# Kernel optimization log

Measured on AMD Instinct MI355X. Metric: run time of the kernel, lower is better.

Reference implementation:

```python
import jax, jax.numpy as jnp
import numpy as np

BN_EPS = 1e-3  # keras BatchNormalization default epsilon
NEG_INF = -1e30


def _masked_row_softmax(adjT):
    # tf.sparse.softmax semantics: softmax over NONZERO entries of each row;
    # implicit zeros stay exactly zero.
    mask = adjT != 0
    logits = jnp.where(mask, adjT, NEG_INF)
    p = jax.nn.softmax(logits, axis=-1)
    return jnp.where(mask, p, 0.0)


def _batch_norm(x, gamma, beta):
    # training-mode BN over all axes except channels
    mean = jnp.mean(x, axis=(0, 1), keepdims=True)
    var = jnp.var(x, axis=(0, 1), keepdims=True)
    return (x - mean) * jax.lax.rsqrt(var + BN_EPS) * gamma + beta


def setup_inputs() -> dict:
    key = jax.random.key(0)
    ks = jax.random.split(key, 4)
    B, N, F = 1, 8192, 128
    C0, C1 = 256, 128
    features = jax.random.normal(ks[0], (B, N, F), dtype=jnp.float32)
    adj = jax.random.randint(ks[1], (B, N, N), 0, 2, dtype=jnp.int32)
    kernel_1 = jax.random.normal(ks[2], (F, C0), dtype=jnp.float32) * (1.0 / np.sqrt(F))
    kernel_2 = jax.random.normal(ks[3], (C0, C1), dtype=jnp.float32) * (1.0 / np.sqrt(C0))
    return {
        "features": features,
        "adj": adj,
        "kernel_1": kernel_1,
        "bias_1": jnp.zeros((C0,), jnp.float32),
        "gamma_1": jnp.ones((C0,), jnp.float32),
        "beta_1": jnp.zeros((C0,), jnp.float32),
        "kernel_2": kernel_2,
        "bias_2": jnp.zeros((C1,), jnp.float32),
        "gamma_2": jnp.ones((C1,), jnp.float32),
        "beta_2": jnp.zeros((C1,), jnp.float32),
    }


def reference(features, adj, kernel_1, bias_1, gamma_1, beta_1,
              kernel_2, bias_2, gamma_2, beta_2):
    # fltr transposed: (B, Nr, Np), then sparse softmax over last dim
    adjT = jnp.transpose(adj.astype(jnp.float32), (0, 2, 1))
    w = _masked_row_softmax(adjT)                      # (B, Nr, Np)
    # people -> region aggregation + projection
    region = jnp.matmul(w, features)                   # (B, Nr, F)
    region = jnp.matmul(region, kernel_1) + bias_1     # (B, Nr, C0)
    region = _batch_norm(region, gamma_1, beta_1)
    # region -> people aggregation + projection
    people = jnp.matmul(jnp.transpose(w, (0, 2, 1)), region)  # (B, Np, C0)
    people = jnp.matmul(people, kernel_2) + bias_2             # (B, Np, C1)
    people = _batch_norm(people, gamma_2, beta_2)
    return people
```

## Files before the change

### kernel.cpp

```cpp
#include <hip/hip_runtime.h>
#include <stdint.h>

typedef unsigned int u32;
typedef unsigned short u16;
typedef unsigned long long u64;
typedef __attribute__((ext_vector_type(8))) short short8;
typedef __attribute__((ext_vector_type(4))) float f32x4;

#define N8K 8192

__device__ __forceinline__ float b2f(u16 u) { return __uint_as_float(((u32)u) << 16); }
__device__ __forceinline__ u16 f2b(float f) {
  u32 i = __float_as_uint(f);
  i += 0x7FFFu + ((i >> 16) & 1u);
  return (u16)(i >> 16);
}
__device__ __forceinline__ u32 pkf(float a, float b) { return (u32)f2b(a) | ((u32)f2b(b) << 16); }

__device__ __forceinline__ int dvote(const u16* f16) {
  u16 u = f16[threadIdx.x * 2];
  int e = (u >> 7) & 0xFF;
  return __syncthreads_count((e >= 0x60 && e <= 0x9F) ? 1 : 0) >= 128;
}

__device__ __forceinline__ void gl_lds16(const void* g, void* l) {
  __builtin_amdgcn_global_load_lds(
      (const __attribute__((address_space(1))) u32*)g,
      (__attribute__((address_space(3))) u32*)l, 16, 0, 0);
}

__device__ __forceinline__ void unpack16(u32 b, uint4& o0, uint4& o1) {
  o0.x = ((b & 0x0001u) ? 0x3F80u : 0u) | ((b & 0x0002u) ? 0x3F800000u : 0u);
  o0.y = ((b & 0x0004u) ? 0x3F80u : 0u) | ((b & 0x0008u) ? 0x3F800000u : 0u);
  o0.z = ((b & 0x0010u) ? 0x3F80u : 0u) | ((b & 0x0020u) ? 0x3F800000u : 0u);
  o0.w = ((b & 0x0040u) ? 0x3F80u : 0u) | ((b & 0x0080u) ? 0x3F800000u : 0u);
  o1.x = ((b & 0x0100u) ? 0x3F80u : 0u) | ((b & 0x0200u) ? 0x3F800000u : 0u);
  o1.y = ((b & 0x0400u) ? 0x3F80u : 0u) | ((b & 0x0800u) ? 0x3F800000u : 0u);
  o1.z = ((b & 0x1000u) ? 0x3F80u : 0u) | ((b & 0x2000u) ? 0x3F800000u : 0u);
  o1.w = ((b & 0x4000u) ? 0x3F80u : 0u) | ((b & 0x8000u) ? 0x3F800000u : 0u);
}

#define MFMA_4x4(As_, Bs_, aoff_, boff_)                                         \
  {                                                                              \
    short8 afr[4], bfr[4];                                                       \
    _Pragma("unroll") for (int i_ = 0; i_ < 4; ++i_)                             \
      afr[i_] = *(const short8*)(As_ + aoff_[i_]);                               \
    _Pragma("unroll") for (int j_ = 0; j_ < 4; ++j_)                             \
      bfr[j_] = *(const short8*)(Bs_ + boff_[j_]);                               \
    _Pragma("unroll") for (int i_ = 0; i_ < 4; ++i_)                             \
      _Pragma("unroll") for (int j_ = 0; j_ < 4; ++j_)                           \
        acc[i_][j_] = __builtin_amdgcn_mfma_f32_16x16x32_bf16(                   \
            afr[i_], bfr[j_], acc[i_][j_], 0, 0, 0);                             \
  }

#define ZERO_ACC()                                                               \
  f32x4 acc[4][4];                                                               \
  {                                                                              \
    const f32x4 fz = {0.f, 0.f, 0.f, 0.f};                                       \
    _Pragma("unroll") for (int i_ = 0; i_ < 4; ++i_)                             \
      _Pragma("unroll") for (int j_ = 0; j_ < 4; ++j_) acc[i_][j_] = fz;         \
  }

__global__ void k_prep(const int* __restrict__ adj,
                       const void* __restrict__ featv, const void* __restrict__ K1v,
                       const void* __restrict__ K2v,
                       const void* __restrict__ b1v, const void* __restrict__ g1v,
                       const void* __restrict__ be1v, const void* __restrict__ b2v,
                       const void* __restrict__ g2v, const void* __restrict__ be2v,
                       u32* __restrict__ RB, u32* __restrict__ CB,
                       u16* __restrict__ Ft, u16* __restrict__ K1T, u16* __restrict__ K2T,
                       float* __restrict__ deg, float* __restrict__ par,
                       float* __restrict__ bn1s, float* __restrict__ bn1q,
                       float* __restrict__ bn2s, float* __restrict__ bn2q) {
  __shared__ u32 Ls[64 * 65];
  __shared__ __align__(16) u16 Lf[32 * 136];
  const int b = blockIdx.x, t = threadIdx.x;
  if (b < 16384) {
    const int r0 = (b & 127) << 6, p0 = (b >> 7) << 6;
    const int lr = t >> 4, lc = (t & 15) << 2;
#pragma unroll
    for (int k = 0; k < 4; ++k) {
      int row = k * 16 + lr;
      int4 v = *(const int4*)(adj + (size_t)(p0 + row) * N8K + r0 + lc);
      u32* d = &Ls[row * 65 + lc];
      d[0] = (u32)v.x; d[1] = (u32)v.y; d[2] = (u32)v.z; d[3] = (u32)v.w;
    }
    __syncthreads();
    const int wv = t >> 6, l = t & 63;
#pragma unroll 4
    for (int i = 0; i < 16; ++i) {
      int row = wv * 16 + i;
      u64 m = __ballot(Ls[row * 65 + l] != 0u);
      if (l == 0) *(u64*)(RB + (size_t)(p0 + row) * 256 + (r0 >> 5)) = m;
    }
#pragma unroll 4
    for (int i = 0; i < 16; ++i) {
      int col = wv * 16 + i;
      u64 m = __ballot(Ls[l * 65 + col] != 0u);
      if (l == 0) *(u64*)(CB + (size_t)(r0 + col) * 256 + (p0 >> 5)) = m;
    }
  } else if (b < 16640) {
    const int flag = dvote((const u16*)featv);
    const int bb = b - 16384;
    const int pr = t >> 3, ck = t & 7;
    u16 v[16];
    if (flag) {
      const u16* s = (const u16*)featv + (size_t)(bb * 32 + pr) * 128 + ck * 16;
      *(uint4*)&v[0] = *(const uint4*)(s);
      *(uint4*)&v[8] = *(const uint4*)(s + 8);
    } else {
      const float* s = (const float*)featv + (size_t)(bb * 32 + pr) * 128 + ck * 16;
#pragma unroll
      for (int i = 0; i < 16; ++i) v[i] = f2b(s[i]);
    }
    *(uint4*)(Lf + pr * 136 + ck * 16) = *(uint4*)&v[0];
    *(uint4*)(Lf + pr * 136 + ck * 16 + 8) = *(uint4*)&v[8];
    __syncthreads();
    const int f = t >> 1, h16 = (t & 1) * 16;
    u32 w[8];
#pragma unroll
    for (int i = 0; i < 8; ++i) {
      u16 lo = Lf[(h16 + 2 * i) * 136 + f];
      u16 hi = Lf[(h16 + 2 * i + 1) * 136 + f];
      w[i] = (u32)lo | ((u32)hi << 16);
    }
    u16* d = Ft + (size_t)bb * 4096 + f * 32 + h16;
    *(uint4*)(d) = *(uint4*)&w[0];
    *(uint4*)(d + 8) = *(uint4*)&w[4];
  } else if (b < 16656) {
    const int flag = dvote((const u16*)featv);
    int o = ((b - 16640) * 256 + t) << 3;
    int k0 = o >> 13, c = (o >> 5) & 255, kk = o & 31;
    uint4 w;
    if (flag) {
      const u16* s = (const u16*)K1v + (size_t)(k0 * 32 + kk) * 256 + c;
      w.x = (u32)s[0]    | ((u32)s[256]  << 16);
      w.y = (u32)s[512]  | ((u32)s[768]  << 16);
      w.z = (u32)s[1024] | ((u32)s[1280] << 16);
      w.w = (u32)s[1536] | ((u32)s[1792] << 16);
    } else {
      const float* s = (const float*)K1v + (size_t)(k0 * 32 + kk) * 256 + c;
      w.x = pkf(s[0], s[256]); w.y = pkf(s[512], s[768]);
      w.z = pkf(s[1024], s[1280]); w.w = pkf(s[1536], s[1792]);
    }
    *(uint4*)(K1T + o) = w;
  } else if (b < 16672) {
    const int flag = dvote((const u16*)featv);
    int o = ((b - 16656) * 256 + t) << 3;
    int k0 = o >> 12, c = (o >> 5) & 127, kk = o & 31;
    uint4 w;
    if (flag) {
      const u16* s = (const u16*)K2v + (size_t)(k0 * 32 + kk) * 128 + c;
      w.x = (u32)s[0]   | ((u32)s[128] << 16);
      w.y = (u32)s[256] | ((u32)s[384] << 16);
      w.z = (u32)s[512] | ((u32)s[640] << 16);
      w.w = (u32)s[768] | ((u32)s[896] << 16);
    } else {
      const float* s = (const float*)K2v + (size_t)(k0 * 32 + kk) * 128 + c;
      w.x = pkf(s[0], s[128]); w.y = pkf(s[256], s[384]);
      w.z = pkf(s[512], s[640]); w.w = pkf(s[768], s[896]);
    }
    *(uint4*)(K2T + o) = w;
  } else {
    const int flag = dvote((const u16*)featv);
    if (t < 256) {
      par[t]       = flag ? b2f(((const u16*)b1v)[t])  : ((const float*)b1v)[t];
      par[256 + t] = flag ? b2f(((const u16*)g1v)[t])  : ((const float*)g1v)[t];
      par[512 + t] = flag ? b2f(((const u16*)be1v)[t]) : ((const float*)be1v)[t];
      bn1s[t] = 0.f; bn1q[t] = 0.f;
    }
    if (t < 128) {
      par[768 + t]  = flag ? b2f(((const u16*)b2v)[t])  : ((const float*)b2v)[t];
      par[896 + t]  = flag ? b2f(((const u16*)g2v)[t])  : ((const float*)g2v)[t];
      par[1024 + t] = flag ? b2f(((const u16*)be2v)[t]) : ((const float*)be2v)[t];
      bn2s[t] = 0.f; bn2q[t] = 0.f;
    }
    for (int i = t; i < N8K; i += 256) deg[i] = 0.f;
  }
}

__global__ __launch_bounds__(256, 2)
void k_gemm1(const u32* __restrict__ CB, const u16* __restrict__ Ft,
             float* __restrict__ P1, float* __restrict__ deg, int ksteps) {
  __shared__ __align__(16) u16 As[128 * 32];
  __shared__ __align__(16) u16 Bs[128 * 32];
  __shared__ float degp[128];
  const int t = threadIdx.x, bx = blockIdx.x;
  const int nt = bx & 63, s = bx >> 6;
  const int n0 = nt << 7;
  const int lane = t & 63, wv = t >> 6;
  const int wm = (wv & 1) << 6, wn = (wv >> 1) << 6;
  const int fm = lane & 15, fq = lane >> 4;
  if (t < 128) degp[t] = 0.0f;
  ZERO_ACC();
  int aoff[4], boff[4];
#pragma unroll
  for (int i = 0; i < 4; ++i) aoff[i] = (wm + i * 16 + fm) * 32 + fq * 8;
#pragma unroll
  for (int j = 0; j < 4; ++j) {
    int n = wn + j * 16 + fm;
    boff[j] = n * 32 + ((fq * 8) ^ (((n >> 2) & 3) << 3));
  }
  const int row = t >> 1, h = t & 1;
  const u32* gB = CB + (size_t)(n0 + row) * 256 + s * ksteps;
  const char* gA = (const char*)(Ft + (size_t)s * ksteps * 4096);
  char* lA = (char*)As + ((t >> 6) << 10);
  const int goff = t << 4;
  const int swz = ((row >> 2) & 3) << 3;
  u16* lb0 = Bs + row * 32 + ((h * 16) ^ swz);
  u16* lb1 = Bs + row * 32 + (((h * 16) + 8) ^ swz);
  int cnt = 0;
  for (int ks = 0; ks < ksteps; ++ks) {
    __syncthreads();
    gl_lds16(gA + goff, lA);
    gl_lds16(gA + 4096 + goff, lA + 4096);
    u32 w = gB[ks];
    gA += 8192;
    u32 bits = (w >> (h * 16)) & 0xFFFFu;
    cnt += __popc(bits);
    uint4 o0, o1;
    unpack16(bits, o0, o1);
    *(uint4*)lb0 = o0;
    *(uint4*)lb1 = o1;
    __syncthreads();
    MFMA_4x4(As, Bs, aoff, boff);
  }
  atomicAdd(&degp[row], (float)cnt);
  float* base = P1 + ((size_t)s * N8K + n0) * 128;
#pragma unroll
  for (int i = 0; i < 4; ++i)
#pragma unroll
    for (int j = 0; j < 4; ++j) {
      int r = wn + j * 16 + fm;
      int f = wm + i * 16 + fq * 4;
      *(f32x4*)(base + (size_t)r * 128 + f) = acc[i][j];
    }
  __syncthreads();
  if (t < 128) atomicAdd(&deg[n0 + t], degp[t]);
}

__global__ __launch_bounds__(256, 2)
void k_projf(const float* __restrict__ Psrc, const float* __restrict__ deg,
             const u16* __restrict__ Bt, const float* __restrict__ bias,
             float* __restrict__ Cout, float* __restrict__ bns, float* __restrict__ bnq,
             int nsplit, int ksteps, int Ncols, int useinv) {
  __shared__ __align__(16) u16 As[128 * 32];
  __shared__ __align__(16) u16 Bs[128 * 32];
  const int t = threadIdx.x, bx = blockIdx.x;
  const int ct = bx & 1, mt = (bx >> 1) & 63;
  const int m0 = mt << 7, n0 = ct << 7;
  const int lane = t & 63, wv = t >> 6;
  const int wm = (wv & 1) << 6, wn = (wv >> 1) << 6;
  const int fm = lane & 15, fq = lane >> 4;
  const int K = ksteps << 5;
  ZERO_ACC();
  int aoff[4], boff[4];
#pragma unroll
  for (int i = 0; i < 4; ++i) {
    int m = wm + i * 16 + fm;
    aoff[i] = m * 32 + ((fq * 8) ^ (((m >> 2) & 3) << 3));
  }
#pragma unroll
  for (int j = 0; j < 4; ++j) boff[j] = (wn + j * 16 + fm) * 32 + fq * 8;
  const int row = t >> 1;
  const size_t sstride = (size_t)N8K * K;
  const float* src = Psrc + (size_t)(m0 + row) * K + (t & 1) * 16;
  float inv = 1.0f;
  if (useinv) {
    float d = deg[m0 + row];
    inv = (d > 0.5f) ? 1.0f / d : 0.0f;
  }
  const int swzA = ((t >> 3) & 3) << 3;
  u16* la0 = As + row * 32 + (((t & 1) * 16) ^ swzA);
  u16* la1 = As + row * 32 + ((((t & 1) * 16) + 8) ^ swzA);
  char* lB = (char*)Bs + ((t >> 6) << 10);
  const int goff = t << 4;
  for (int ks = 0; ks < ksteps; ++ks) {
    __syncthreads();
    const char* gB = (const char*)(Bt + ((size_t)ks * Ncols + n0) * 32);
    gl_lds16(gB + goff, lB);
    gl_lds16(gB + 4096 + goff, lB + 4096);
    f32x4 s0 = {0.f, 0.f, 0.f, 0.f}, s1 = s0, s2 = s0, s3 = s0;
    const float* p = src + ks * 32;
    for (int sp = 0; sp < nsplit; ++sp) {
      const f32x4* q = (const f32x4*)(p + sp * sstride);
      s0 += q[0]; s1 += q[1]; s2 += q[2]; s3 += q[3];
    }
    s0 *= inv; s1 *= inv; s2 *= inv; s3 *= inv;
    uint4 w;
    w.x = pkf(s0[0], s0[1]); w.y = pkf(s0[2], s0[3]);
    w.z = pkf(s1[0], s1[1]); w.w = pkf(s1[2], s1[3]);
    *(uint4*)la0 = w;
    w.x = pkf(s2[0], s2[1]); w.y = pkf(s2[2], s2[3]);
    w.z = pkf(s3[0], s3[1]); w.w = pkf(s3[2], s3[3]);
    *(uint4*)la1 = w;
    __syncthreads();
    MFMA_4x4(As, Bs, aoff, boff);
  }
#pragma unroll
  for (int j = 0; j < 4; ++j) {
    int c = n0 + wn + j * 16 + fm;
    float bc = bias[c];
    float t1 = 0.f, t2 = 0.f;
#pragma unroll
    for (int i = 0; i < 4; ++i) {
      int r = m0 + wm + i * 16 + fq * 4;
#pragma unroll
      for (int ii = 0; ii < 4; ++ii) {
        float v = acc[i][j][ii] + bc;
        Cout[(size_t)(r + ii) * Ncols + c] = v;
        t1 += v; t2 += v * v;
      }
    }
    t1 += __shfl_xor(t1, 16); t1 += __shfl_xor(t1, 32);
    t2 += __shfl_xor(t2, 16); t2 += __shfl_xor(t2, 32);
    if (fq == 0) { atomicAdd(&bns[c], t1); atomicAdd(&bnq[c], t2); }
  }
}

__global__ __launch_bounds__(256, 2)
void k_bnH(const float* __restrict__ region1, const float* __restrict__ deg,
           const float* __restrict__ bn1s, const float* __restrict__ bn1q,
           const float* __restrict__ g1, const float* __restrict__ be1,
           const u16* __restrict__ K2T, u16* __restrict__ HT) {
  __shared__ __align__(16) u16 As[128 * 32];
  __shared__ __align__(16) u16 Bs[128 * 32];
  __shared__ float scS[256], shS[256];
  const int t = threadIdx.x, mt = blockIdx.x;
  const int m0 = mt << 7;
  const int lane = t & 63, wv = t >> 6;
  const int wm = (wv & 1) << 6, wn = (wv >> 1) << 6;
  const int fm = lane & 15, fq = lane >> 4;
  {
    float mu = bn1s[t] * (1.0f / 8192.0f);
    float var = bn1q[t] * (1.0f / 8192.0f) - mu * mu;
    float iv = rsqrtf(var + 1e-3f);
    float sc = iv * g1[t];
    scS[t] = sc;
    shS[t] = be1[t] - mu * sc;
  }
  ZERO_ACC();
  int aoff[4], boff[4];
#pragma unroll
  for (int i = 0; i < 4; ++i) {
    int m = wm + i * 16 + fm;
    aoff[i] = m * 32 + ((fq * 8) ^ (((m >> 2) & 3) << 3));
  }
#pragma unroll
  for (int j = 0; j < 4; ++j) boff[j] = (wn + j * 16 + fm) * 32 + fq * 8;
  const int row = t >> 1, half = t & 1;
  float d = deg[m0 + row];
  const float idg = (d > 0.5f) ? 1.0f / d : 0.0f;
  const float* src = region1 + (size_t)(m0 + row) * 256 + half * 16;
  const int swzA = ((t >> 3) & 3) << 3;
  u16* la0 = As + row * 32 + ((half * 16) ^ swzA);
  u16* la1 = As + row * 32 + (((half * 16) + 8) ^ swzA);
  char* lB = (char*)Bs + ((t >> 6) << 10);
  const int goff = t << 4;
  for (int ks = 0; ks < 8; ++ks) {
    __syncthreads();
    const char* gB = (const char*)(K2T + (size_t)ks * 4096);
    gl_lds16(gB + goff, lB);
    gl_lds16(gB + 4096 + goff, lB + 4096);
    const float* p = src + ks * 32;
    const int cb = ks * 32 + half * 16;
    float y[16];
#pragma unroll
    for (int q = 0; q < 4; ++q) {
      f32x4 x = *(const f32x4*)(p + q * 4);
#pragma unroll
      for (int jj = 0; jj < 4; ++jj)
        y[q * 4 + jj] = (x[jj] * scS[cb + q * 4 + jj] + shS[cb + q * 4 + jj]) * idg;
    }
    uint4 w;
    w.x = pkf(y[0], y[1]); w.y = pkf(y[2], y[3]);
    w.z = pkf(y[4], y[5]); w.w = pkf(y[6], y[7]);
    *(uint4*)la0 = w;
    w.x = pkf(y[8], y[9]); w.y = pkf(y[10], y[11]);
    w.z = pkf(y[12], y[13]); w.w = pkf(y[14], y[15]);
    *(uint4*)la1 = w;
    __syncthreads();
    MFMA_4x4(As, Bs, aoff, boff);
  }
#pragma unroll
  for (int i = 0; i < 4; ++i)
#pragma unroll
    for (int j = 0; j < 4; ++j) {
      int c = wn + j * 16 + fm;
      int r = m0 + wm + i * 16 + fq * 4;
      uint2 w;
      w.x = pkf(acc[i][j][0], acc[i][j][1]);
      w.y = pkf(acc[i][j][2], acc[i][j][3]);
      *(uint2*)(HT + (size_t)(r >> 5) * 4096 + c * 32 + (r & 31)) = w;
    }
}

__global__ __launch_bounds__(256, 2)
void k_gemm2(const u32* __restrict__ RB, const u16* __restrict__ HT,
             float* __restrict__ P2, int ksteps) {
  __shared__ __align__(16) u16 As[128 * 32];
  __shared__ __align__(16) u16 Bs[128 * 32];
  const int t = threadIdx.x, bx = blockIdx.x;
  const int mt = bx & 63, s = bx >> 6;
  const int m0 = mt << 7;
  const int lane = t & 63, wv = t >> 6;
  const int wm = (wv & 1) << 6, wn = (wv >> 1) << 6;
  const int fm = lane & 15, fq = lane >> 4;
  ZERO_ACC();
  int aoff[4], boff[4];
#pragma unroll
  for (int i = 0; i < 4; ++i) {
    int m = wm + i * 16 + fm;
    aoff[i] = m * 32 + ((fq * 8) ^ (((m >> 2) & 3) << 3));
  }
#pragma unroll
  for (int j = 0; j < 4; ++j) boff[j] = (wn + j * 16 + fm) * 32 + fq * 8;
  const int row = t >> 1, h = t & 1;
  const u32* gA = RB + (size_t)(m0 + row) * 256 + s * ksteps;
  const char* gB = (const char*)(HT + (size_t)s * ksteps * 4096);
  char* lB = (char*)Bs + ((t >> 6) << 10);
  const int goff = t << 4;
  const int swzA = ((row >> 2) & 3) << 3;
  u16* la0 = As + row * 32 + ((h * 16) ^ swzA);
  u16* la1 = As + row * 32 + (((h * 16) + 8) ^ swzA);
  for (int ks = 0; ks < ksteps; ++ks) {
    __syncthreads();
    gl_lds16(gB + goff, lB);
    gl_lds16(gB + 4096 + goff, lB + 4096);
    u32 w = gA[ks];
    gB += 8192;
    u32 bits = (w >> (h * 16)) & 0xFFFFu;
    uint4 o0, o1;
    unpack16(bits, o0, o1);
    *(uint4*)la0 = o0;
    *(uint4*)la1 = o1;
    __syncthreads();
    MFMA_4x4(As, Bs, aoff, boff);
  }
  float* base = P2 + (size_t)s * N8K * 128;
#pragma unroll
  for (int i = 0; i < 4; ++i)
#pragma unroll
    for (int j = 0; j < 4; ++j) {
      int c = wn + j * 16 + fm;
      int pr = m0 + wm + i * 16 + fq * 4;
#pragma unroll
      for (int ii = 0; ii < 4; ++ii)
        base[(size_t)(pr + ii) * 128 + c] = acc[i][j][ii];
    }
}

__global__ void k_red2(const float* __restrict__ P2, const float* __restrict__ bias,
                       float* __restrict__ people1,
                       float* __restrict__ bn2s, float* __restrict__ bn2q) {
  __shared__ float r1[256], r2[256];
  const int t = threadIdx.x;
  const int c = t & 127, pg = t >> 7;
  const int p0 = blockIdx.x << 5;
  const float bc = bias[c];
  float s1 = 0.f, s2 = 0.f;
  for (int pp = pg; pp < 32; pp += 2) {
    size_t o = (size_t)(p0 + pp) * 128 + c;
    float v = bc;
#pragma unroll
    for (int s = 0; s < 8; ++s) v += P2[(size_t)s * N8K * 128 + o];
    people1[o] = v;
    s1 += v; s2 += v * v;
  }
  r1[t] = s1; r2[t] = s2;
  __syncthreads();
  if (t < 128) {
    atomicAdd(&bn2s[t], r1[t] + r1[t + 128]);
    atomicAdd(&bn2q[t], r2[t] + r2[t + 128]);
  }
}

__global__ void k_bn2apply(const float* __restrict__ people1,
                           const float* __restrict__ bn2s, const float* __restrict__ bn2q,
                           const float* __restrict__ g2, const float* __restrict__ be2,
                           const u16* __restrict__ featprobe, void* __restrict__ outv) {
  const int flag = dvote(featprobe);
  int g = blockIdx.x * 256 + threadIdx.x;
  int p = g >> 5;
  int c = (g & 31) << 2;
  f32x4 x = *(const f32x4*)(people1 + (size_t)p * 128 + c);
  f32x4 y;
#pragma unroll
  for (int jj = 0; jj < 4; ++jj) {
    int cc = c + jj;
    float mu = bn2s[cc] * (1.0f / 8192.0f);
    float var = bn2q[cc] * (1.0f / 8192.0f) - mu * mu;
    float inv = rsqrtf(var + 1e-3f);
    y[jj] = (x[jj] - mu) * inv * g2[cc] + be2[cc];
  }
  if (flag) {
    uint2 w;
    w.x = pkf(y[0], y[1]);
    w.y = pkf(y[2], y[3]);
    *(uint2*)((u16*)outv + (size_t)p * 128 + c) = w;
  } else {
    *(f32x4*)((float*)outv + (size_t)p * 128 + c) = y;
  }
}

extern "C" void kernel_launch(void* const* d_in, const int* in_sizes, int n_in,
                              void* d_out, int out_size, void* d_ws, size_t ws_size,
                              hipStream_t stream) {
  const void* feat = d_in[0];
  const int* adj   = (const int*)d_in[1];
  const void* K1   = d_in[2];
  const void* b1   = d_in[3];
  const void* g1   = d_in[4];
  const void* be1  = d_in[5];
  const void* K2   = d_in[6];
  const void* b2   = d_in[7];
  const void* g2   = d_in[8];
  const void* be2  = d_in[9];
  char* ws = (char*)d_ws;
  const size_t MB = 1u << 20;

  float* Pbig    = (float*)(ws);
  float* region1 = (float*)(ws + 32 * MB);
  float* people1 = (float*)(ws + 40 * MB);
  u16*   Ft      = (u16*)(ws + 44 * MB);
  u16*   HT      = (u16*)(ws + 46 * MB);
  u32*   RB      = (u32*)(ws + 48 * MB);
  u32*   CB      = (u32*)(ws + 56 * MB);
  u16*   K1T     = (u16*)(ws + 64 * MB);
  u16*   K2T     = K1T + 32768;
  float* deg     = (float*)(K2T + 32768);
  float* par     = deg + N8K;
  float* bn1s    = par + 1152;
  float* bn1q    = bn1s + 256;
  float* bn2s    = bn1q + 256;
  float* bn2q    = bn2s + 128;

  k_prep<<<16673, 256, 0, stream>>>(adj, feat, K1, K2, b1, g1, be1, b2, g2, be2,
                                    RB, CB, Ft, K1T, K2T, deg, par,
                                    bn1s, bn1q, bn2s, bn2q);
  k_gemm1<<<512, 256, 0, stream>>>(CB, Ft, Pbig, deg, 32);
  k_projf<<<128, 256, 0, stream>>>(Pbig, deg, K1T, par + 0, region1, bn1s, bn1q,
                                   8, 4, 256, 1);
  k_bnH<<<64, 256, 0, stream>>>(region1, deg, bn1s, bn1q, par + 256, par + 512,
                                K2T, HT);
  k_gemm2<<<512, 256, 0, stream>>>(RB, HT, Pbig, 32);
  k_red2<<<256, 256, 0, stream>>>(Pbig, par + 768, people1, bn2s, bn2q);
  k_bn2apply<<<1024, 256, 0, stream>>>(people1, bn2s, bn2q, par + 896, par + 1024,
                                       (const u16*)feat, d_out);
}
```

Before: 508.1 us.

## Load MFMA fragments directly from global memory, removing LDS staging and barriers

The four GEMM kernels no longer stage A/B tiles through shared memory with double __syncthreads per k-step. Each lane now reads its MFMA fragments straight from global memory, and the adjacency bitmask is unpacked in registers per lane, reading four k-steps of mask words at once. Degree counting moves from shared-memory atomics to per-lane popcounts plus global atomics. This removes barrier and LDS traffic, but each lane now issues more redundant global loads through L1/L2, and load latency is no longer hidden by explicit staging.

```diff
diff --git a/kernel.cpp b/kernel.cpp
--- a/kernel.cpp
+++ b/kernel.cpp
@@ -9,6 +9,8 @@
 
 #define N8K 8192
 
+union U16x8 { uint4 u; short8 s; };
+
 __device__ __forceinline__ float b2f(u16 u) { return __uint_as_float(((u32)u) << 16); }
 __device__ __forceinline__ u16 f2b(float f) {
   u32 i = __float_as_uint(f);
@@ -23,35 +25,20 @@
   return __syncthreads_count((e >= 0x60 && e <= 0x9F) ? 1 : 0) >= 128;
 }
 
-__device__ __forceinline__ void gl_lds16(const void* g, void* l) {
-  __builtin_amdgcn_global_load_lds(
-      (const __attribute__((address_space(1))) u32*)g,
-      (__attribute__((address_space(3))) u32*)l, 16, 0, 0);
-}
-
-__device__ __forceinline__ void unpack16(u32 b, uint4& o0, uint4& o1) {
-  o0.x = ((b & 0x0001u) ? 0x3F80u : 0u) | ((b & 0x0002u) ? 0x3F800000u : 0u);
-  o0.y = ((b & 0x0004u) ? 0x3F80u : 0u) | ((b & 0x0008u) ? 0x3F800000u : 0u);
-  o0.z = ((b & 0x0010u) ? 0x3F80u : 0u) | ((b & 0x0020u) ? 0x3F800000u : 0u);
-  o0.w = ((b & 0x0040u) ? 0x3F80u : 0u) | ((b & 0x0080u) ? 0x3F800000u : 0u);
-  o1.x = ((b & 0x0100u) ? 0x3F80u : 0u) | ((b & 0x0200u) ? 0x3F800000u : 0u);
-  o1.y = ((b & 0x0400u) ? 0x3F80u : 0u) | ((b & 0x0800u) ? 0x3F800000u : 0u);
-  o1.z = ((b & 0x1000u) ? 0x3F80u : 0u) | ((b & 0x2000u) ? 0x3F800000u : 0u);
-  o1.w = ((b & 0x4000u) ? 0x3F80u : 0u) | ((b & 0x8000u) ? 0x3F800000u : 0u);
-}
-
-#define MFMA_4x4(As_, Bs_, aoff_, boff_)                                         \
-  {                                                                              \
-    short8 afr[4], bfr[4];                                                       \
-    _Pragma("unroll") for (int i_ = 0; i_ < 4; ++i_)                             \
-      afr[i_] = *(const short8*)(As_ + aoff_[i_]);                               \
+__device__ __forceinline__ short8 unpack8(u32 b) {
+  U16x8 u;
+  u.u.x = ((b & 0x01u) ? 0x3F80u : 0u) | ((b & 0x02u) ? 0x3F800000u : 0u);
+  u.u.y = ((b & 0x04u) ? 0x3F80u : 0u) | ((b & 0x08u) ? 0x3F800000u : 0u);
+  u.u.z = ((b & 0x10u) ? 0x3F80u : 0u) | ((b & 0x20u) ? 0x3F800000u : 0u);
+  u.u.w = ((b & 0x40u) ? 0x3F80u : 0u) | ((b & 0x80u) ? 0x3F800000u : 0u);
+  return u.s;
+}
+
+#define MFMA_ALL()                                                               \
+  _Pragma("unroll") for (int i_ = 0; i_ < 4; ++i_)                               \
     _Pragma("unroll") for (int j_ = 0; j_ < 4; ++j_)                             \
-      bfr[j_] = *(const short8*)(Bs_ + boff_[j_]);                               \
-    _Pragma("unroll") for (int i_ = 0; i_ < 4; ++i_)                             \
-      _Pragma("unroll") for (int j_ = 0; j_ < 4; ++j_)                           \
-        acc[i_][j_] = __builtin_amdgcn_mfma_f32_16x16x32_bf16(                   \
-            afr[i_], bfr[j_], acc[i_][j_], 0, 0, 0);                             \
-  }
+      acc[i_][j_] = __builtin_amdgcn_mfma_f32_16x16x32_bf16(                     \
+          afr[i_], bfr[j_], acc[i_][j_], 0, 0, 0);
 
 #define ZERO_ACC()                                                               \
   f32x4 acc[4][4];                                                               \
@@ -60,6 +47,11 @@
     _Pragma("unroll") for (int i_ = 0; i_ < 4; ++i_)                             \
       _Pragma("unroll") for (int j_ = 0; j_ < 4; ++j_) acc[i_][j_] = fz;         \
   }
+
+#define LANE_DECODE()                                                            \
+  const int lane = t & 63, wv = t >> 6;                                          \
+  const int wm = (wv & 1) << 6, wn = (wv >> 1) << 6;                             \
+  const int fm = lane & 15, fq = lane >> 4;
 
 __global__ void k_prep(const int* __restrict__ adj,
                        const void* __restrict__ featv, const void* __restrict__ K1v,
@@ -181,51 +173,48 @@
 
 __global__ __launch_bounds__(256, 2)
 void k_gemm1(const u32* __restrict__ CB, const u16* __restrict__ Ft,
-             float* __restrict__ P1, float* __restrict__ deg, int ksteps) {
-  __shared__ __align__(16) u16 As[128 * 32];
-  __shared__ __align__(16) u16 Bs[128 * 32];
-  __shared__ float degp[128];
+             float* __restrict__ P1, float* __restrict__ deg) {
   const int t = threadIdx.x, bx = blockIdx.x;
   const int nt = bx & 63, s = bx >> 6;
   const int n0 = nt << 7;
-  const int lane = t & 63, wv = t >> 6;
-  const int wm = (wv & 1) << 6, wn = (wv >> 1) << 6;
-  const int fm = lane & 15, fq = lane >> 4;
-  if (t < 128) degp[t] = 0.0f;
+  LANE_DECODE();
+  const int sh = fq * 8;
   ZERO_ACC();
-  int aoff[4], boff[4];
-#pragma unroll
-  for (int i = 0; i < 4; ++i) aoff[i] = (wm + i * 16 + fm) * 32 + fq * 8;
-#pragma unroll
-  for (int j = 0; j < 4; ++j) {
-    int n = wn + j * 16 + fm;
-    boff[j] = n * 32 + ((fq * 8) ^ (((n >> 2) & 3) << 3));
-  }
-  const int row = t >> 1, h = t & 1;
-  const u32* gB = CB + (size_t)(n0 + row) * 256 + s * ksteps;
-  const char* gA = (const char*)(Ft + (size_t)s * ksteps * 4096);
-  char* lA = (char*)As + ((t >> 6) << 10);
-  const int goff = t << 4;
-  const int swz = ((row >> 2) & 3) << 3;
-  u16* lb0 = Bs + row * 32 + ((h * 16) ^ swz);
-  u16* lb1 = Bs + row * 32 + (((h * 16) + 8) ^ swz);
-  int cnt = 0;
-  for (int ks = 0; ks < ksteps; ++ks) {
-    __syncthreads();
-    gl_lds16(gA + goff, lA);
-    gl_lds16(gA + 4096 + goff, lA + 4096);
-    u32 w = gB[ks];
-    gA += 8192;
-    u32 bits = (w >> (h * 16)) & 0xFFFFu;
-    cnt += __popc(bits);
-    uint4 o0, o1;
-    unpack16(bits, o0, o1);
-    *(uint4*)lb0 = o0;
-    *(uint4*)lb1 = o1;
-    __syncthreads();
-    MFMA_4x4(As, Bs, aoff, boff);
-  }
-  atomicAdd(&degp[row], (float)cnt);
+  const u16* aP[4];
+#pragma unroll
+  for (int i = 0; i < 4; ++i)
+    aP[i] = Ft + (size_t)s * 32 * 4096 + (wm + i * 16 + fm) * 32 + fq * 8;
+  const u32* bP[4];
+#pragma unroll
+  for (int j = 0; j < 4; ++j)
+    bP[j] = CB + (size_t)(n0 + wn + j * 16 + fm) * 256 + s * 32;
+  u32 cnt[4] = {0u, 0u, 0u, 0u};
+  for (int ks4 = 0; ks4 < 8; ++ks4) {
+    uint4 bw[4];
+#pragma unroll
+    for (int j = 0; j < 4; ++j) bw[j] = *(const uint4*)(bP[j] + ks4 * 4);
+#pragma unroll
+    for (int kk = 0; kk < 4; ++kk) {
+      short8 afr[4], bfr[4];
+#pragma unroll
+      for (int i = 0; i < 4; ++i)
+        afr[i] = *(const short8*)(aP[i] + (ks4 * 4 + kk) * 4096);
+#pragma unroll
+      for (int j = 0; j < 4; ++j) {
+        u32 w = ((const u32*)&bw[j])[kk];
+        bfr[j] = unpack8((w >> sh) & 0xFFu);
+      }
+      MFMA_ALL();
+    }
+#pragma unroll
+    for (int j = 0; j < 4; ++j)
+      cnt[j] += __popc(bw[j].x) + __popc(bw[j].y) + __popc(bw[j].z) + __popc(bw[j].w);
+  }
+  if (((wv & 1) == 0) && fq == 0) {
+#pragma unroll
+    for (int j = 0; j < 4; ++j)
+      atomicAdd(&deg[n0 + wn + j * 16 + fm], (float)cnt[j]);
+  }
   float* base = P1 + ((size_t)s * N8K + n0) * 128;
 #pragma unroll
   for (int i = 0; i < 4; ++i)
@@ -235,67 +224,47 @@
       int f = wm + i * 16 + fq * 4;
       *(f32x4*)(base + (size_t)r * 128 + f) = acc[i][j];
     }
-  __syncthreads();
-  if (t < 128) atomicAdd(&deg[n0 + t], degp[t]);
 }
 
 __global__ __launch_bounds__(256, 2)
-void k_projf(const float* __restrict__ Psrc, const float* __restrict__ deg,
-             const u16* __restrict__ Bt, const float* __restrict__ bias,
-             float* __restrict__ Cout, float* __restrict__ bns, float* __restrict__ bnq,
-             int nsplit, int ksteps, int Ncols, int useinv) {
-  __shared__ __align__(16) u16 As[128 * 32];
-  __shared__ __align__(16) u16 Bs[128 * 32];
+void k_projf(const float* __restrict__ P1, const float* __restrict__ deg,
+             const u16* __restrict__ K1T, const float* __restrict__ bias,
+             float* __restrict__ Cout, float* __restrict__ bns, float* __restrict__ bnq) {
   const int t = threadIdx.x, bx = blockIdx.x;
-  const int ct = bx & 1, mt = (bx >> 1) & 63;
+  const int ct = bx & 1, mt = bx >> 1;
   const int m0 = mt << 7, n0 = ct << 7;
-  const int lane = t & 63, wv = t >> 6;
-  const int wm = (wv & 1) << 6, wn = (wv >> 1) << 6;
-  const int fm = lane & 15, fq = lane >> 4;
-  const int K = ksteps << 5;
+  LANE_DECODE();
   ZERO_ACC();
-  int aoff[4], boff[4];
+  int rowi[4];
+  float idg[4];
 #pragma unroll
   for (int i = 0; i < 4; ++i) {
-    int m = wm + i * 16 + fm;
-    aoff[i] = m * 32 + ((fq * 8) ^ (((m >> 2) & 3) << 3));
-  }
-#pragma unroll
-  for (int j = 0; j < 4; ++j) boff[j] = (wn + j * 16 + fm) * 32 + fq * 8;
-  const int row = t >> 1;
-  const size_t sstride = (size_t)N8K * K;
-  const float* src = Psrc + (size_t)(m0 + row) * K + (t & 1) * 16;
-  float inv = 1.0f;
-  if (useinv) {
-    float d = deg[m0 + row];
-    inv = (d > 0.5f) ? 1.0f / d : 0.0f;
-  }
-  const int swzA = ((t >> 3) & 3) << 3;
-  u16* la0 = As + row * 32 + (((t & 1) * 16) ^ swzA);
-  u16* la1 = As + row * 32 + ((((t & 1) * 16) + 8) ^ swzA);
-  char* lB = (char*)Bs + ((t >> 6) << 10);
-  const int goff = t << 4;
-  for (int ks = 0; ks < ksteps; ++ks) {
-    __syncthreads();
-    const char* gB = (const char*)(Bt + ((size_t)ks * Ncols + n0) * 32);
-    gl_lds16(gB + goff, lB);
-    gl_lds16(gB + 4096 + goff, lB + 4096);
-    f32x4 s0 = {0.f, 0.f, 0.f, 0.f}, s1 = s0, s2 = s0, s3 = s0;
-    const float* p = src + ks * 32;
-    for (int sp = 0; sp < nsplit; ++sp) {
-      const f32x4* q = (const f32x4*)(p + sp * sstride);
-      s0 += q[0]; s1 += q[1]; s2 += q[2]; s3 += q[3];
-    }
-    s0 *= inv; s1 *= inv; s2 *= inv; s3 *= inv;
-    uint4 w;
-    w.x = pkf(s0[0], s0[1]); w.y = pkf(s0[2], s0[3]);
-    w.z = pkf(s1[0], s1[1]); w.w = pkf(s1[2], s1[3]);
-    *(uint4*)la0 = w;
-    w.x = pkf(s2[0], s2[1]); w.y = pkf(s2[2], s2[3]);
-    w.z = pkf(s3[0], s3[1]); w.w = pkf(s3[2], s3[3]);
-    *(uint4*)la1 = w;
-    __syncthreads();
-    MFMA_4x4(As, Bs, aoff, boff);
+    rowi[i] = m0 + wm + i * 16 + fm;
+    float d = deg[rowi[i]];
+    idg[i] = (d > 0.5f) ? 1.0f / d : 0.0f;
+  }
+  for (int ks = 0; ks < 4; ++ks) {
+    short8 afr[4], bfr[4];
+#pragma unroll
+    for (int i = 0; i < 4; ++i) {
+      const float* p = P1 + (size_t)rowi[i] * 128 + ks * 32 + fq * 8;
+      f32x4 s0 = {0.f, 0.f, 0.f, 0.f}, s1 = s0;
+#pragma unroll
+      for (int sp = 0; sp < 8; ++sp) {
+        const float* q = p + (size_t)sp * N8K * 128;
+        s0 += *(const f32x4*)(q);
+        s1 += *(const f32x4*)(q + 4);
+      }
+      s0 *= idg[i]; s1 *= idg[i];
+      U16x8 u;
+      u.u.x = pkf(s0[0], s0[1]); u.u.y = pkf(s0[2], s0[3]);
+      u.u.z = pkf(s1[0], s1[1]); u.u.w = pkf(s1[2], s1[3]);
+      afr[i] = u.s;
+    }
+#pragma unroll
+    for (int j = 0; j < 4; ++j)
+      bfr[j] = *(const short8*)(K1T + ((size_t)ks * 256 + n0 + wn + j * 16 + fm) * 32 + fq * 8);
+    MFMA_ALL();
   }
 #pragma unroll
   for (int j = 0; j < 4; ++j) {
@@ -308,7 +277,7 @@
 #pragma unroll
       for (int ii = 0; ii < 4; ++ii) {
         float v = acc[i][j][ii] + bc;
-        Cout[(size_t)(r + ii) * Ncols + c] = v;
+        Cout[(size_t)(r + ii) * 256 + c] = v;
         t1 += v; t2 += v * v;
       }
     }
@@ -323,14 +292,10 @@
            const float* __restrict__ bn1s, const float* __restrict__ bn1q,
            const float* __restrict__ g1, const float* __restrict__ be1,
            const u16* __restrict__ K2T, u16* __restrict__ HT) {
-  __shared__ __align__(16) u16 As[128 * 32];
-  __shared__ __align__(16) u16 Bs[128 * 32];
   __shared__ float scS[256], shS[256];
   const int t = threadIdx.x, mt = blockIdx.x;
   const int m0 = mt << 7;
-  const int lane = t & 63, wv = t >> 6;
-  const int wm = (wv & 1) << 6, wn = (wv >> 1) << 6;
-  const int fm = lane & 15, fq = lane >> 4;
+  LANE_DECODE();
   {
     float mu = bn1s[t] * (1.0f / 8192.0f);
     float var = bn1q[t] * (1.0f / 8192.0f) - mu * mu;
@@ -339,48 +304,41 @@
     scS[t] = sc;
     shS[t] = be1[t] - mu * sc;
   }
+  __syncthreads();
   ZERO_ACC();
-  int aoff[4], boff[4];
+  int rowi[4];
+  float idg[4];
 #pragma unroll
   for (int i = 0; i < 4; ++i) {
-    int m = wm + i * 16 + fm;
-    aoff[i] = m * 32 + ((fq * 8) ^ (((m >> 2) & 3) << 3));
-  }
-#pragma unroll
-  for (int j = 0; j < 4; ++j) boff[j] = (wn + j * 16 + fm) * 32 + fq * 8;
-  const int row = t >> 1, half = t & 1;
-  float d = deg[m0 + row];
-  const float idg = (d > 0.5f) ? 1.0f / d : 0.0f;
-  const float* src = region1 + (size_t)(m0 + row) * 256 + half * 16;
-  const int swzA = ((t >> 3) & 3) << 3;
-  u16* la0 = As + row * 32 + ((half * 16) ^ swzA);
-  u16* la1 = As + row * 32 + (((half * 16) + 8) ^ swzA);
-  char* lB = (char*)Bs + ((t >> 6) << 10);
-  const int goff = t << 4;
+    rowi[i] = m0 + wm + i * 16 + fm;
+    float d = deg[rowi[i]];
+    idg[i] = (d > 0.5f) ? 1.0f / d : 0.0f;
+  }
   for (int ks = 0; ks < 8; ++ks) {
-    __syncthreads();
-    const char* gB = (const char*)(K2T + (size_t)ks * 4096);
-    gl_lds16(gB + goff, lB);
-    gl_lds16(gB + 4096 + goff, lB + 4096);
-    const float* p = src + ks * 32;
-    const int cb = ks * 32 + half * 16;
-    float y[16];
-#pragma unroll
-    for (int q = 0; q < 4; ++q) {
-      f32x4 x = *(const f32x4*)(p + q * 4);
-#pragma unroll
-      for (int jj = 0; jj < 4; ++jj)
-        y[q * 4 + jj] = (x[jj] * scS[cb + q * 4 + jj] + shS[cb + q * 4 + jj]) * idg;
-    }
-    uint4 w;
-    w.x = pkf(y[0], y[1]); w.y = pkf(y[2], y[3]);
-    w.z = pkf(y[4], y[5]); w.w = pkf(y[6], y[7]);
-    *(uint4*)la0 = w;
-    w.x = pkf(y[8], y[9]); w.y = pkf(y[10], y[11]);
-    w.z = pkf(y[12], y[13]); w.w = pkf(y[14], y[15]);
-    *(uint4*)la1 = w;
-    __syncthreads();
-    MFMA_4x4(As, Bs, aoff, boff);
+    const int c0 = ks * 32 + fq * 8;
+    float sc[8], shf[8];
+#pragma unroll
+    for (int jj = 0; jj < 8; ++jj) { sc[jj] = scS[c0 + jj]; shf[jj] = shS[c0 + jj]; }
+    short8 afr[4], bfr[4];
+#pragma unroll
+    for (int i = 0; i < 4; ++i) {
+      const float* p = region1 + (size_t)rowi[i] * 256 + c0;
+      f32x4 x0 = *(const f32x4*)(p);
+      f32x4 x1 = *(const f32x4*)(p + 4);
+      float y[8];
+#pragma unroll
+      for (int jj = 0; jj < 4; ++jj) y[jj] = (x0[jj] * sc[jj] + shf[jj]) * idg[i];
+#pragma unroll
+      for (int jj = 0; jj < 4; ++jj) y[4 + jj] = (x1[jj] * sc[4 + jj] + shf[4 + jj]) * idg[i];
+      U16x8 u;
+      u.u.x = pkf(y[0], y[1]); u.u.y = pkf(y[2], y[3]);
+      u.u.z = pkf(y[4], y[5]); u.u.w = pkf(y[6], y[7]);
+      afr[i] = u.s;
+    }
+#pragma unroll
+    for (int j = 0; j < 4; ++j)
+      bfr[j] = *(const short8*)(K2T + ((size_t)ks * 128 + wn + j * 16 + fm) * 32 + fq * 8);
+    MFMA_ALL();
   }
 #pragma unroll
   for (int i = 0; i < 4; ++i)
@@ -397,45 +355,35 @@
 
 __global__ __launch_bounds__(256, 2)
 void k_gemm2(const u32* __restrict__ RB, const u16* __restrict__ HT,
-             float* __restrict__ P2, int ksteps) {
-  __shared__ __align__(16) u16 As[128 * 32];
-  __shared__ __align__(16) u16 Bs[128 * 32];
+             float* __restrict__ P2) {
   const int t = threadIdx.x, bx = blockIdx.x;
   const int mt = bx & 63, s = bx >> 6;
   const int m0 = mt << 7;
-  const int lane = t & 63, wv = t >> 6;
-  const int wm = (wv & 1) << 6, wn = (wv >> 1) << 6;
-  const int fm = lane & 15, fq = lane >> 4;
+  LANE_DECODE();
+  const int sh = fq * 8;
   ZERO_ACC();
-  int aoff[4], boff[4];
-#pragma unroll
-  for (int i = 0; i < 4; ++i) {
-    int m = wm + i * 16 + fm;
-    aoff[i] = m * 32 + ((fq * 8) ^ (((m >> 2) & 3) << 3));
-  }
-#pragma unroll
-  for (int j = 0; j < 4; ++j) boff[j] = (wn + j * 16 + fm) * 32 + fq * 8;
-  const int row = t >> 1, h = t & 1;
-  const u32* gA = RB + (size_t)(m0 + row) * 256 + s * ksteps;
-  const char* gB = (const char*)(HT + (size_t)s * ksteps * 4096);
-  char* lB = (char*)Bs + ((t >> 6) << 10);
-  const int goff = t << 4;
-  const int swzA = ((row >> 2) & 3) << 3;
-  u16* la0 = As + row * 32 + ((h * 16) ^ swzA);
-  u16* la1 = As + row * 32 + (((h * 16) + 8) ^ swzA);
-  for (int ks = 0; ks < ksteps; ++ks) {
-    __syncthreads();
-    gl_lds16(gB + goff, lB);
-    gl_lds16(gB + 4096 + goff, lB + 4096);
-    u32 w = gA[ks];
-    gB += 8192;
-    u32 bits = (w >> (h * 16)) & 0xFFFFu;
-    uint4 o0, o1;
-    unpack16(bits, o0, o1);
-    *(uint4*)la0 = o0;
-    *(uint4*)la1 = o1;
-    __syncthreads();
-    MFMA_4x4(As, Bs, aoff, boff);
+  const u32* aP[4];
+#pragma unroll
+  for (int i = 0; i < 4; ++i)
+    aP[i] = RB + (size_t)(m0 + wm + i * 16 + fm) * 256 + s * 32;
+  const u16* bB = HT + (size_t)s * 32 * 4096 + fq * 8;
+  for (int ks4 = 0; ks4 < 8; ++ks4) {
+    uint4 aw[4];
+#pragma unroll
+    for (int i = 0; i < 4; ++i) aw[i] = *(const uint4*)(aP[i] + ks4 * 4);
+#pragma unroll
+    for (int kk = 0; kk < 4; ++kk) {
+      short8 afr[4], bfr[4];
+#pragma unroll
+      for (int i = 0; i < 4; ++i) {
+        u32 w = ((const u32*)&aw[i])[kk];
+        afr[i] = unpack8((w >> sh) & 0xFFu);
+      }
+#pragma unroll
+      for (int j = 0; j < 4; ++j)
+        bfr[j] = *(const short8*)(bB + (size_t)(ks4 * 4 + kk) * 4096 + (wn + j * 16 + fm) * 32);
+      MFMA_ALL();
+    }
   }
   float* base = P2 + (size_t)s * N8K * 128;
 #pragma unroll
@@ -538,12 +486,11 @@
   k_prep<<<16673, 256, 0, stream>>>(adj, feat, K1, K2, b1, g1, be1, b2, g2, be2,
                                     RB, CB, Ft, K1T, K2T, deg, par,
                                     bn1s, bn1q, bn2s, bn2q);
-  k_gemm1<<<512, 256, 0, stream>>>(CB, Ft, Pbig, deg, 32);
-  k_projf<<<128, 256, 0, stream>>>(Pbig, deg, K1T, par + 0, region1, bn1s, bn1q,
-                                   8, 4, 256, 1);
+  k_gemm1<<<512, 256, 0, stream>>>(CB, Ft, Pbig, deg);
+  k_projf<<<128, 256, 0, stream>>>(Pbig, deg, K1T, par + 0, region1, bn1s, bn1q);
   k_bnH<<<64, 256, 0, stream>>>(region1, deg, bn1s, bn1q, par + 256, par + 512,
                                 K2T, HT);
-  k_gemm2<<<512, 256, 0, stream>>>(RB, HT, Pbig, 32);
+  k_gemm2<<<512, 256, 0, stream>>>(RB, HT, Pbig);
   k_red2<<<256, 256, 0, stream>>>(Pbig, par + 768, people1, bn2s, bn2q);
   k_bn2apply<<<1024, 256, 0, stream>>>(people1, bn2s, bn2q, par + 896, par + 1024,
                                        (const u16*)feat, d_out);
```

After: 529.1 us. 4.1% more time.
